# Performance work log

Hardware: AMD Instinct MI355X
Metric: run time of the kernel (lower is better)

The kernel has to match this reference:

```python
import jax, jax.numpy as jnp
import numpy as np

D_MODEL, N_HEADS, N_GROUPS, BASE = 2048, 32, 8, 10000
HEAD_DIM = D_MODEL // N_HEADS  # 64


def _rope_cache(seq, head_dim, base=BASE):
    half = head_dim // 2
    theta = 1.0 / (base ** (jnp.arange(0, head_dim, 2)[:half].astype(jnp.float32) / head_dim))
    ang = jnp.einsum('i,j->ij', jnp.arange(seq, dtype=jnp.float32), theta)  # (seq, half)
    return jnp.cos(ang), jnp.sin(ang)


def _apply_rope(x):
    # x: (b, s, h, head_dim) -> interleaved-pair rotation, matching torch module
    b, s, h, hd = x.shape
    cos, sin = _rope_cache(s, hd)
    xr = x.reshape(b, s, h, hd // 2, 2)
    c = cos[None, :, None, :]
    sn = sin[None, :, None, :]
    x0, x1 = xr[..., 0], xr[..., 1]
    out = jnp.stack((x0 * c - x1 * sn, x1 * c + x0 * sn), axis=-1)
    return out.reshape(b, s, h, hd).astype(x.dtype)


def setup_inputs() -> dict:
    key = jax.random.key(0)
    ks = jax.random.split(key, 8)
    B, S = 1, 2048
    kv_dim = HEAD_DIM * N_GROUPS
    return {
        'Q': jax.random.normal(ks[0], (B, S, D_MODEL), jnp.float32),
        'K': jax.random.normal(ks[1], (B, S, D_MODEL), jnp.float32),
        'V': jax.random.normal(ks[2], (B, S, D_MODEL), jnp.float32),
        'attention_mask': jnp.ones((B, S), jnp.int32),
        'Wq': jax.random.normal(ks[3], (D_MODEL, D_MODEL), jnp.float32) * 0.02,
        'Wk': jax.random.normal(ks[4], (D_MODEL, kv_dim), jnp.float32) * 0.02,
        'Wv': jax.random.normal(ks[5], (D_MODEL, kv_dim), jnp.float32) * 0.02,
        'Wo': jax.random.normal(ks[6], (D_MODEL, D_MODEL), jnp.float32) * 0.02,
        'bo': jnp.zeros((D_MODEL,), jnp.float32),
    }


def reference(Q, K, V, attention_mask, Wq, Wk, Wv, Wo, bo):
    b, s, _ = Q.shape
    g, hpg, hd = N_GROUPS, N_HEADS // N_GROUPS, HEAD_DIM
    # projections (weights stored as [in, out], equivalent to torch x @ W.T)
    q = (Q @ Wq).reshape(b, s, N_HEADS, hd)
    q = _apply_rope(q).reshape(b, s, g, hpg, hd)
    k = _apply_rope((K @ Wk).reshape(b, s, g, hd))
    v = (V @ Wv).reshape(b, s, g, hd)

    scale = jnp.sqrt(jnp.float32(hd))
    scores = jnp.einsum('bnghd,bmgd->bnghm', q, k) / scale  # (b, s, g, hpg, s)
    # padding mask (b, 1, 1, 1, s) and causal mask (1, s, 1, 1, s)
    pad = (attention_mask != 0)[:, None, None, None, :]
    causal = jnp.tril(jnp.ones((s, s), bool))[None, :, None, None, :]
    scores = jnp.where(pad & causal, scores, -jnp.inf)
    attn = jax.nn.softmax(scores, axis=-1)  # dropout p=0.0 -> identity
    out = jnp.einsum('bnghm,bmgd->bnghd', attn, v).reshape(b, s, D_MODEL)
    return out @ Wo + bo
```

## Files before the change

kernel.cpp:

```cpp
#include <hip/hip_runtime.h>

typedef __bf16 bf16_t;
typedef __bf16 bf16x8 __attribute__((ext_vector_type(8)));
typedef __bf16 bf16x4 __attribute__((ext_vector_type(4)));
typedef __bf16 bf16x2 __attribute__((ext_vector_type(2)));
typedef float  f32x4  __attribute__((ext_vector_type(4)));

#define LOG2E 1.44269504088896340736f

__global__ __launch_bounds__(256) void rope_table_k(float* __restrict__ cs,
                                                    float* __restrict__ sn, int S) {
  int i = blockIdx.x * 256 + threadIdx.x;
  if (i >= S * 32) return;
  int s = i >> 5, j = i & 31;
  float theta = powf(10000.0f, -(float)j * (1.0f / 32.0f));
  float a = (float)s * theta;
  cs[i] = cosf(a);
  sn[i] = sinf(a);
}

__global__ __launch_bounds__(256) void cast3_k(const float* __restrict__ A,
                                               const float* __restrict__ B,
                                               const float* __restrict__ C,
                                               bf16_t* __restrict__ oa,
                                               bf16_t* __restrict__ ob,
                                               bf16_t* __restrict__ oc) {
  const int b = blockIdx.x;
  const float* in; bf16_t* out;
  if (b < 2048) { in = A; out = oa; }
  else if (b < 4096) { in = B; out = ob; }
  else { in = C; out = oc; }
  const int j = (b & 2047) * 256 + threadIdx.x;
  const float4 v0 = *(const float4*)&in[(size_t)j * 8];
  const float4 v1 = *(const float4*)&in[(size_t)j * 8 + 4];
  bf16x8 o;
  o[0]=(bf16_t)v0.x; o[1]=(bf16_t)v0.y; o[2]=(bf16_t)v0.z; o[3]=(bf16_t)v0.w;
  o[4]=(bf16_t)v1.x; o[5]=(bf16_t)v1.y; o[6]=(bf16_t)v1.z; o[7]=(bf16_t)v1.w;
  *(bf16x8*)&out[(size_t)j * 8] = o;
}

__global__ void transpose_cast_k(const float* __restrict__ in, bf16_t* __restrict__ out,
                                 int R, int C) {
  __shared__ float tile[32][33];
  int c0 = blockIdx.x * 32, r0 = blockIdx.y * 32;
  int tx = threadIdx.x, ty = threadIdx.y;
  #pragma unroll
  for (int k = 0; k < 32; k += 8)
    tile[ty + k][tx] = in[(size_t)(r0 + ty + k) * C + c0 + tx];
  __syncthreads();
  #pragma unroll
  for (int k = 0; k < 32; k += 8)
    out[(size_t)(c0 + ty + k) * R + r0 + tx] = (bf16_t)tile[tx][ty + k];
}

__device__ __forceinline__ int xcd_swz(int bid, int nb) {
  const int q = nb >> 3, r = nb & 7;
  const int xcd = bid & 7, idx = bid >> 3;
  return (xcd < r ? xcd * (q + 1) : r * (q + 1) + (xcd - r) * q) + idx;
}

__global__ __launch_bounds__(256) void gemm2_k(
    const bf16_t* __restrict__ Aq, const bf16_t* __restrict__ Ak, const bf16_t* __restrict__ Av,
    const bf16_t* __restrict__ Bq, const bf16_t* __restrict__ Bk, const bf16_t* __restrict__ Bv,
    const int K, const int N, const int mode,
    const float* __restrict__ cs, const float* __restrict__ sn,
    bf16_t* __restrict__ oq, bf16_t* __restrict__ okg, bf16_t* __restrict__ ovt,
    float* __restrict__ ofp, const float* __restrict__ bias, const int S,
    const int ncb, const int nb) {
  __shared__ bf16_t a_lds[64][72];
  __shared__ bf16_t b_lds[128][72];
  const int tid = threadIdx.x;
  const int wid = tid >> 6, lane = tid & 63;
  const int fr = lane & 15, kg = lane >> 4;

  const int lin = xcd_swz(blockIdx.x, nb);
  const int cb = lin % ncb, rb = lin / ncb;
  const bf16_t* Ap; const bf16_t* Bp; int emode, col0;
  if (mode == 3) { Ap = Aq; Bp = Bq; emode = 3; col0 = cb * 128; }
  else if (cb < 16) { Ap = Aq; Bp = Bq; emode = 0; col0 = cb * 128; }
  else if (cb < 20) { Ap = Ak; Bp = Bk; emode = 1; col0 = (cb - 16) * 128; }
  else              { Ap = Av; Bp = Bv; emode = 2; col0 = (cb - 20) * 128; }
  const int row0 = rb * 64;
  const int wr = (wid >> 1) * 32, wc = (wid & 1) * 64;

  f32x4 acc[2][4];
  #pragma unroll
  for (int i = 0; i < 2; ++i)
    #pragma unroll
    for (int j = 0; j < 4; ++j)
      acc[i][j] = (f32x4){0.f, 0.f, 0.f, 0.f};

  const int ra = tid >> 2, sa = (tid & 3) * 16;
  const int rbv = tid >> 1, sb = (tid & 1) * 32;

  bf16x8 a0, a1, b0, b1, b2, b3;

#define LOADA(kt)                                                              \
  do {                                                                         \
    const bf16_t* p = &Ap[(size_t)(row0 + ra) * K + (kt) + sa];                \
    a0 = *(const bf16x8*)(p); a1 = *(const bf16x8*)(p + 8);                    \
    const bf16_t* q = &Bp[(size_t)(col0 + rbv) * K + (kt) + sb];               \
    b0 = *(const bf16x8*)(q);      b1 = *(const bf16x8*)(q + 8);               \
    b2 = *(const bf16x8*)(q + 16); b3 = *(const bf16x8*)(q + 24);              \
  } while (0)

  LOADA(0);

  for (int kt = 0; kt < K; kt += 64) {
    __syncthreads();
    *(bf16x8*)&a_lds[ra][sa]      = a0;
    *(bf16x8*)&a_lds[ra][sa + 8]  = a1;
    *(bf16x8*)&b_lds[rbv][sb]      = b0;
    *(bf16x8*)&b_lds[rbv][sb + 8]  = b1;
    *(bf16x8*)&b_lds[rbv][sb + 16] = b2;
    *(bf16x8*)&b_lds[rbv][sb + 24] = b3;
    __syncthreads();
    if (kt + 64 < K) LOADA(kt + 64);
    #pragma unroll
    for (int ks = 0; ks < 2; ++ks) {
      bf16x8 af[2], bfr[4];
      #pragma unroll
      for (int mi = 0; mi < 2; ++mi) af[mi]  = *(const bf16x8*)&a_lds[wr + mi * 16 + fr][ks * 32 + kg * 8];
      #pragma unroll
      for (int ni = 0; ni < 4; ++ni) bfr[ni] = *(const bf16x8*)&b_lds[wc + ni * 16 + fr][ks * 32 + kg * 8];
      #pragma unroll
      for (int mi = 0; mi < 2; ++mi)
        #pragma unroll
        for (int ni = 0; ni < 4; ++ni)
          acc[mi][ni] = __builtin_amdgcn_mfma_f32_16x16x32_bf16(af[mi], bfr[ni], acc[mi][ni], 0, 0, 0);
    }
  }
#undef LOADA

  #pragma unroll
  for (int mi = 0; mi < 2; ++mi) {
    #pragma unroll
    for (int ni = 0; ni < 4; ++ni) {
      #pragma unroll
      for (int r = 0; r < 4; ++r) {
        const int grow = row0 + wr + mi * 16 + kg * 4 + r;
        const int gcol = col0 + wc + ni * 16 + fr;
        float v = acc[mi][ni][r];
        if (emode == 3) {
          ofp[(size_t)grow * N + gcol] = v + bias[gcol];
        } else if (emode == 2) {
          const int gi = gcol >> 6, d = gcol & 63;
          ovt[((size_t)gi * 64 + d) * S + grow] = (bf16_t)v;
        } else {
          const float pv = __shfl_xor(v, 1);
          const int d = gcol & 63, p = d >> 1, hh = gcol >> 6;
          const float c = cs[grow * 32 + p], s = sn[grow * 32 + p];
          float o = (d & 1) ? fmaf(pv, s, v * c) : fmaf(-pv, s, v * c);
          if (emode == 0) {
            o *= 0.125f * LOG2E;
            oq[((size_t)hh * S + grow) * 64 + d] = (bf16_t)o;
          } else {
            okg[((size_t)hh * S + grow) * 64 + d] = (bf16_t)o;
          }
        }
      }
    }
  }
}

__device__ __forceinline__ int swz8(int r, int c) { return r * 64 + (((c) ^ (r & 7)) << 3); }

__global__ __launch_bounds__(256) void attn_k(
    const bf16_t* __restrict__ qh,
    const bf16_t* __restrict__ kgr,
    const bf16_t* __restrict__ vtg,
    const int* __restrict__ amask,
    bf16_t* __restrict__ ao,
    const int S) {
  __shared__ bf16_t k_lds[64 * 64];
  __shared__ bf16_t vt_lds[64 * 64];
  __shared__ bf16_t p_lds[4][16 * 64];
  const int tid = threadIdx.x, wid = tid >> 6, lane = tid & 63;
  const int fr = lane & 15, kgp = lane >> 4;
  const int h = blockIdx.x, g = h >> 2;
  const int qb = 31 - blockIdx.y;
  const int q0 = qb * 64 + wid * 16;
  const int qg = q0 + fr;

  const bf16_t* qbase = qh + ((size_t)h * S + q0 + fr) * 64;
  const bf16x8 qf0 = *(const bf16x8*)&qbase[kgp * 8];
  const bf16x8 qf1 = *(const bf16x8*)&qbase[32 + kgp * 8];

  f32x4 oacc[4];
  #pragma unroll
  for (int t = 0; t < 4; ++t) oacc[t] = (f32x4){0.f, 0.f, 0.f, 0.f};
  float m_ = -1e30f, l_ = 0.f;

  const int srow = tid >> 2, sc4 = tid & 3;
  const bf16_t* kbase = kgr + (size_t)g * S * 64;
  const bf16_t* vbase = vtg + (size_t)g * 64 * S;
  const int cmax = qb + 1;

  bf16x8 nk0 = *(const bf16x8*)&kbase[(size_t)srow * 64 + sc4 * 8];
  bf16x8 nk1 = *(const bf16x8*)&kbase[(size_t)srow * 64 + 32 + sc4 * 8];
  bf16x8 nv0 = *(const bf16x8*)&vbase[(size_t)srow * S + sc4 * 8];
  bf16x8 nv1 = *(const bf16x8*)&vbase[(size_t)srow * S + 32 + sc4 * 8];
  int mvc = amask[lane];
  *(bf16x8*)&k_lds[swz8(srow, sc4)]      = nk0;
  *(bf16x8*)&k_lds[swz8(srow, 4 + sc4)]  = nk1;
  *(bf16x8*)&vt_lds[swz8(srow, sc4)]     = nv0;
  *(bf16x8*)&vt_lds[swz8(srow, 4 + sc4)] = nv1;
  __syncthreads();

  for (int c = 0; c < cmax; ++c) {
    const int kc0 = c * 64;
    const unsigned long long pm = __ballot(mvc == 0);
    const bool more = (c + 1 < cmax);
    if (more) {
      const int kc1 = kc0 + 64;
      nk0 = *(const bf16x8*)&kbase[(size_t)(kc1 + srow) * 64 + sc4 * 8];
      nk1 = *(const bf16x8*)&kbase[(size_t)(kc1 + srow) * 64 + 32 + sc4 * 8];
      nv0 = *(const bf16x8*)&vbase[(size_t)srow * S + kc1 + sc4 * 8];
      nv1 = *(const bf16x8*)&vbase[(size_t)srow * S + kc1 + 32 + sc4 * 8];
      mvc = amask[kc1 + lane];
    }

    f32x4 sc[4];
    #pragma unroll
    for (int a = 0; a < 4; ++a) {
      const bf16x8 ka0 = *(const bf16x8*)&k_lds[swz8(a * 16 + fr, kgp)];
      const bf16x8 ka1 = *(const bf16x8*)&k_lds[swz8(a * 16 + fr, 4 + kgp)];
      f32x4 z = (f32x4){0.f, 0.f, 0.f, 0.f};
      z = __builtin_amdgcn_mfma_f32_16x16x32_bf16(ka0, qf0, z, 0, 0, 0);
      z = __builtin_amdgcn_mfma_f32_16x16x32_bf16(ka1, qf1, z, 0, 0, 0);
      sc[a] = z;
    }

    if (c == qb) {
      #pragma unroll
      for (int a = 0; a < 4; ++a)
        #pragma unroll
        for (int r = 0; r < 4; ++r) {
          const int kl = a * 16 + 4 * kgp + r;
          if (kc0 + kl > qg) sc[a][r] = -1e30f;
        }
    }
    if (pm) {
      #pragma unroll
      for (int a = 0; a < 4; ++a)
        #pragma unroll
        for (int r = 0; r < 4; ++r) {
          const int kl = a * 16 + 4 * kgp + r;
          if ((pm >> kl) & 1) sc[a][r] = -1e30f;
        }
    }

    float smax = sc[0][0];
    #pragma unroll
    for (int a = 0; a < 4; ++a)
      #pragma unroll
      for (int r = 0; r < 4; ++r) smax = fmaxf(smax, sc[a][r]);
    smax = fmaxf(smax, __shfl_xor(smax, 16));
    smax = fmaxf(smax, __shfl_xor(smax, 32));
    const float mn = fmaxf(m_, smax);
    const float al = exp2f(m_ - mn);
    float ps = 0.f;
    #pragma unroll
    for (int a = 0; a < 4; ++a)
      #pragma unroll
      for (int r = 0; r < 4; ++r) {
        const float p = exp2f(sc[a][r] - mn);
        sc[a][r] = p;
        ps += p;
      }
    ps += __shfl_xor(ps, 16);
    ps += __shfl_xor(ps, 32);
    l_ = l_ * al + ps;
    m_ = mn;
    #pragma unroll
    for (int t = 0; t < 4; ++t)
      #pragma unroll
      for (int r = 0; r < 4; ++r) oacc[t][r] *= al;

    #pragma unroll
    for (int a = 0; a < 4; ++a)
      #pragma unroll
      for (int j = 0; j < 2; ++j) {
        bf16x2 w;
        w[0] = (bf16_t)sc[a][2 * j];
        w[1] = (bf16_t)sc[a][2 * j + 1];
        const int off = a * 16 + 4 * kgp + 2 * j;
        *(bf16x2*)&p_lds[wid][fr * 64 + (((off >> 3) ^ (fr & 7)) << 3) + (off & 7)] = w;
      }
    const bf16x8 pa0 = *(const bf16x8*)&p_lds[wid][swz8(fr, kgp)];
    const bf16x8 pa1 = *(const bf16x8*)&p_lds[wid][swz8(fr, 4 + kgp)];

    #pragma unroll
    for (int t = 0; t < 4; ++t) {
      const bf16x8 vb0 = *(const bf16x8*)&vt_lds[swz8(t * 16 + fr, kgp)];
      const bf16x8 vb1 = *(const bf16x8*)&vt_lds[swz8(t * 16 + fr, 4 + kgp)];
      oacc[t] = __builtin_amdgcn_mfma_f32_16x16x32_bf16(vb0, pa0, oacc[t], 0, 0, 0);
      oacc[t] = __builtin_amdgcn_mfma_f32_16x16x32_bf16(vb1, pa1, oacc[t], 0, 0, 0);
    }

    if (more) {
      __syncthreads();
      *(bf16x8*)&k_lds[swz8(srow, sc4)]      = nk0;
      *(bf16x8*)&k_lds[swz8(srow, 4 + sc4)]  = nk1;
      *(bf16x8*)&vt_lds[swz8(srow, sc4)]     = nv0;
      *(bf16x8*)&vt_lds[swz8(srow, 4 + sc4)] = nv1;
      __syncthreads();
    }
  }

  const float inv = 1.0f / l_;
  #pragma unroll
  for (int t = 0; t < 4; ++t) {
    bf16x4 o4;
    #pragma unroll
    for (int r = 0; r < 4; ++r) o4[r] = (bf16_t)(oacc[t][r] * inv);
    *(bf16x4*)&ao[(size_t)(q0 + fr) * 2048 + h * 64 + t * 16 + 4 * kgp] = o4;
  }
}

extern "C" void kernel_launch(void* const* d_in, const int* in_sizes, int n_in,
                              void* d_out, int out_size, void* d_ws, size_t ws_size,
                              hipStream_t stream) {
  const float* Q  = (const float*)d_in[0];
  const float* K  = (const float*)d_in[1];
  const float* V  = (const float*)d_in[2];
  const int*   am = (const int*)d_in[3];
  const float* Wq = (const float*)d_in[4];
  const float* Wk = (const float*)d_in[5];
  const float* Wv = (const float*)d_in[6];
  const float* Wo = (const float*)d_in[7];
  const float* bo = (const float*)d_in[8];
  float* out = (float*)d_out;

  const int S = 2048, D = 2048, KV = 512;
  char* w = (char*)d_ws;
  const size_t MB = 1u << 20;
  bf16_t* WqT = (bf16_t*)(w + 0 * MB);
  bf16_t* WoT = (bf16_t*)(w + 8 * MB);
  bf16_t* WkT = (bf16_t*)(w + 16 * MB);
  bf16_t* WvT = (bf16_t*)(w + 18 * MB);
  bf16_t* qh  = (bf16_t*)(w + 20 * MB);
  bf16_t* kgr = (bf16_t*)(w + 28 * MB);
  bf16_t* vtg = (bf16_t*)(w + 30 * MB);
  bf16_t* ao  = (bf16_t*)(w + 32 * MB);
  bf16_t* Qb  = (bf16_t*)(w + 40 * MB);
  bf16_t* Kb  = (bf16_t*)(w + 48 * MB);
  bf16_t* Vb  = (bf16_t*)(w + 56 * MB);
  float*  cs  = (float*)(w + 64 * MB);
  float*  sn  = (float*)(w + 64 * MB + 256 * 1024);

  rope_table_k<<<256, 256, 0, stream>>>(cs, sn, S);
  cast3_k<<<6144, 256, 0, stream>>>(Q, K, V, Qb, Kb, Vb);
  dim3 tb(32, 8);
  transpose_cast_k<<<dim3(64, 64), tb, 0, stream>>>(Wq, WqT, D, D);
  transpose_cast_k<<<dim3(16, 64), tb, 0, stream>>>(Wk, WkT, D, KV);
  transpose_cast_k<<<dim3(16, 64), tb, 0, stream>>>(Wv, WvT, D, KV);
  transpose_cast_k<<<dim3(64, 64), tb, 0, stream>>>(Wo, WoT, D, D);

  gemm2_k<<<768, 256, 0, stream>>>(Qb, Kb, Vb, WqT, WkT, WvT, D, D, 5,
                                   cs, sn, qh, kgr, vtg, nullptr, nullptr, S, 24, 768);

  attn_k<<<dim3(32, 32), 256, 0, stream>>>(qh, kgr, vtg, am, ao, S);

  gemm2_k<<<512, 256, 0, stream>>>(ao, nullptr, nullptr, WoT, nullptr, nullptr,
                                   D, D, 3, nullptr, nullptr, nullptr, nullptr,
                                   nullptr, out, bo, S, 16, 512);
}
```

Before: 162.1 us.

## Use 128x128 tiles for QKV projection, supertile block mapping, merge weight transposes

The fused QKV projection now uses 128x128 output tiles with 4x4 MFMA fragments per wave, which halves the block count and raises operand reuse per LDS load. Both GEMMs map blocks through a 4x4 supertile order with serpentine traversal after XCD swizzling, to improve L2 locality. The output projection gets its own specialised kernel, and the four weight transposes are merged into one launch. The larger tiles raise register and LDS use and leave fewer blocks to fill the CUs.

```diff
diff --git a/kernel.cpp b/kernel.cpp
--- a/kernel.cpp
+++ b/kernel.cpp
@@ -39,10 +39,19 @@
   *(bf16x8*)&out[(size_t)j * 8] = o;
 }
 
-__global__ void transpose_cast_k(const float* __restrict__ in, bf16_t* __restrict__ out,
-                                 int R, int C) {
+__global__ void transpose4_k(const float* __restrict__ Wq, const float* __restrict__ Wk,
+                             const float* __restrict__ Wv, const float* __restrict__ Wo,
+                             bf16_t* __restrict__ WqT, bf16_t* __restrict__ WkT,
+                             bf16_t* __restrict__ WvT, bf16_t* __restrict__ WoT) {
   __shared__ float tile[32][33];
-  int c0 = blockIdx.x * 32, r0 = blockIdx.y * 32;
+  const int bx = blockIdx.x;
+  const float* in; bf16_t* out; int C, cbl;
+  if (bx < 64)      { in = Wq; out = WqT; C = 2048; cbl = bx; }
+  else if (bx < 80) { in = Wk; out = WkT; C = 512;  cbl = bx - 64; }
+  else if (bx < 96) { in = Wv; out = WvT; C = 512;  cbl = bx - 80; }
+  else              { in = Wo; out = WoT; C = 2048; cbl = bx - 96; }
+  const int R = 2048;
+  int c0 = cbl * 32, r0 = blockIdx.y * 32;
   int tx = threadIdx.x, ty = threadIdx.y;
   #pragma unroll
   for (int k = 0; k < 32; k += 8)
@@ -54,86 +63,89 @@
 }
 
 __device__ __forceinline__ int xcd_swz(int bid, int nb) {
-  const int q = nb >> 3, r = nb & 7;
-  const int xcd = bid & 7, idx = bid >> 3;
-  return (xcd < r ? xcd * (q + 1) : r * (q + 1) + (xcd - r) * q) + idx;
-}
-
-__global__ __launch_bounds__(256) void gemm2_k(
+  const int q = nb >> 3;
+  return (bid & 7) * q + (bid >> 3);
+}
+__device__ __forceinline__ void st_map(int lin, int nstc, int& rb, int& cb) {
+  const int stid = lin >> 4, w = lin & 15;
+  const int sr = stid / nstc, t = stid - sr * nstc;
+  const int sc = (sr & 1) ? (nstc - 1 - t) : t;
+  rb = sr * 4 + (w >> 2);
+  cb = sc * 4 + (w & 3);
+}
+
+__global__ __launch_bounds__(256) void gemm128_k(
     const bf16_t* __restrict__ Aq, const bf16_t* __restrict__ Ak, const bf16_t* __restrict__ Av,
     const bf16_t* __restrict__ Bq, const bf16_t* __restrict__ Bk, const bf16_t* __restrict__ Bv,
-    const int K, const int N, const int mode,
-    const float* __restrict__ cs, const float* __restrict__ sn,
-    bf16_t* __restrict__ oq, bf16_t* __restrict__ okg, bf16_t* __restrict__ ovt,
-    float* __restrict__ ofp, const float* __restrict__ bias, const int S,
-    const int ncb, const int nb) {
-  __shared__ bf16_t a_lds[64][72];
+    const int K, const float* __restrict__ cs, const float* __restrict__ sn,
+    bf16_t* __restrict__ oq, bf16_t* __restrict__ okg, bf16_t* __restrict__ ovt, const int S) {
+  __shared__ bf16_t a_lds[128][72];
   __shared__ bf16_t b_lds[128][72];
   const int tid = threadIdx.x;
   const int wid = tid >> 6, lane = tid & 63;
   const int fr = lane & 15, kg = lane >> 4;
 
-  const int lin = xcd_swz(blockIdx.x, nb);
-  const int cb = lin % ncb, rb = lin / ncb;
+  const int lin = xcd_swz(blockIdx.x, 384);
+  int rb, cb; st_map(lin, 6, rb, cb);
   const bf16_t* Ap; const bf16_t* Bp; int emode, col0;
-  if (mode == 3) { Ap = Aq; Bp = Bq; emode = 3; col0 = cb * 128; }
-  else if (cb < 16) { Ap = Aq; Bp = Bq; emode = 0; col0 = cb * 128; }
+  if (cb < 16)      { Ap = Aq; Bp = Bq; emode = 0; col0 = cb * 128; }
   else if (cb < 20) { Ap = Ak; Bp = Bk; emode = 1; col0 = (cb - 16) * 128; }
   else              { Ap = Av; Bp = Bv; emode = 2; col0 = (cb - 20) * 128; }
-  const int row0 = rb * 64;
-  const int wr = (wid >> 1) * 32, wc = (wid & 1) * 64;
-
-  f32x4 acc[2][4];
-  #pragma unroll
-  for (int i = 0; i < 2; ++i)
+  const int row0 = rb * 128;
+  const int wr = (wid >> 1) * 64, wc = (wid & 1) * 64;
+
+  f32x4 acc[4][4];
+  #pragma unroll
+  for (int i = 0; i < 4; ++i)
     #pragma unroll
     for (int j = 0; j < 4; ++j)
       acc[i][j] = (f32x4){0.f, 0.f, 0.f, 0.f};
 
-  const int ra = tid >> 2, sa = (tid & 3) * 16;
-  const int rbv = tid >> 1, sb = (tid & 1) * 32;
-
-  bf16x8 a0, a1, b0, b1, b2, b3;
-
-#define LOADA(kt)                                                              \
+  const int rw = tid >> 1, sg = (tid & 1) * 32;
+  bf16x8 a0, a1, a2, a3, b0, b1, b2, b3;
+
+#define LOADG(kt)                                                              \
   do {                                                                         \
-    const bf16_t* p = &Ap[(size_t)(row0 + ra) * K + (kt) + sa];                \
-    a0 = *(const bf16x8*)(p); a1 = *(const bf16x8*)(p + 8);                    \
-    const bf16_t* q = &Bp[(size_t)(col0 + rbv) * K + (kt) + sb];               \
-    b0 = *(const bf16x8*)(q);      b1 = *(const bf16x8*)(q + 8);               \
-    b2 = *(const bf16x8*)(q + 16); b3 = *(const bf16x8*)(q + 24);              \
+    const bf16_t* p = &Ap[(size_t)(row0 + rw) * K + (kt) + sg];                \
+    a0 = *(const bf16x8*)(p);      a1 = *(const bf16x8*)(p + 8);               \
+    a2 = *(const bf16x8*)(p + 16); a3 = *(const bf16x8*)(p + 24);              \
+    const bf16_t* q2 = &Bp[(size_t)(col0 + rw) * K + (kt) + sg];               \
+    b0 = *(const bf16x8*)(q2);      b1 = *(const bf16x8*)(q2 + 8);             \
+    b2 = *(const bf16x8*)(q2 + 16); b3 = *(const bf16x8*)(q2 + 24);            \
   } while (0)
 
-  LOADA(0);
+  LOADG(0);
 
   for (int kt = 0; kt < K; kt += 64) {
     __syncthreads();
-    *(bf16x8*)&a_lds[ra][sa]      = a0;
-    *(bf16x8*)&a_lds[ra][sa + 8]  = a1;
-    *(bf16x8*)&b_lds[rbv][sb]      = b0;
-    *(bf16x8*)&b_lds[rbv][sb + 8]  = b1;
-    *(bf16x8*)&b_lds[rbv][sb + 16] = b2;
-    *(bf16x8*)&b_lds[rbv][sb + 24] = b3;
+    *(bf16x8*)&a_lds[rw][sg]      = a0;
+    *(bf16x8*)&a_lds[rw][sg + 8]  = a1;
+    *(bf16x8*)&a_lds[rw][sg + 16] = a2;
+    *(bf16x8*)&a_lds[rw][sg + 24] = a3;
+    *(bf16x8*)&b_lds[rw][sg]      = b0;
+    *(bf16x8*)&b_lds[rw][sg + 8]  = b1;
+    *(bf16x8*)&b_lds[rw][sg + 16] = b2;
+    *(bf16x8*)&b_lds[rw][sg + 24] = b3;
     __syncthreads();
-    if (kt + 64 < K) LOADA(kt + 64);
+    if (kt + 64 < K) LOADG(kt + 64);
     #pragma unroll
     for (int ks = 0; ks < 2; ++ks) {
-      bf16x8 af[2], bfr[4];
-      #pragma unroll
-      for (int mi = 0; mi < 2; ++mi) af[mi]  = *(const bf16x8*)&a_lds[wr + mi * 16 + fr][ks * 32 + kg * 8];
+      bf16x8 af[4], bfr[4];
+      #pragma unroll
+      for (int mi = 0; mi < 4; ++mi) af[mi]  = *(const bf16x8*)&a_lds[wr + mi * 16 + fr][ks * 32 + kg * 8];
       #pragma unroll
       for (int ni = 0; ni < 4; ++ni) bfr[ni] = *(const bf16x8*)&b_lds[wc + ni * 16 + fr][ks * 32 + kg * 8];
       #pragma unroll
-      for (int mi = 0; mi < 2; ++mi)
+      for (int mi = 0; mi < 4; ++mi)
         #pragma unroll
         for (int ni = 0; ni < 4; ++ni)
           acc[mi][ni] = __builtin_amdgcn_mfma_f32_16x16x32_bf16(af[mi], bfr[ni], acc[mi][ni], 0, 0, 0);
     }
   }
-#undef LOADA
-
-  #pragma unroll
-  for (int mi = 0; mi < 2; ++mi) {
+#undef LOADG
+
+  #pragma unroll
+  for (int mi = 0; mi < 4; ++mi) {
     #pragma unroll
     for (int ni = 0; ni < 4; ++ni) {
       #pragma unroll
@@ -141,9 +153,7 @@
         const int grow = row0 + wr + mi * 16 + kg * 4 + r;
         const int gcol = col0 + wc + ni * 16 + fr;
         float v = acc[mi][ni][r];
-        if (emode == 3) {
-          ofp[(size_t)grow * N + gcol] = v + bias[gcol];
-        } else if (emode == 2) {
+        if (emode == 2) {
           const int gi = gcol >> 6, d = gcol & 63;
           ovt[((size_t)gi * 64 + d) * S + grow] = (bf16_t)v;
         } else {
@@ -158,6 +168,83 @@
             okg[((size_t)hh * S + grow) * 64 + d] = (bf16_t)o;
           }
         }
+      }
+    }
+  }
+}
+
+__global__ __launch_bounds__(256) void gemm64o_k(
+    const bf16_t* __restrict__ A, const bf16_t* __restrict__ BT,
+    const int K, const int N,
+    float* __restrict__ ofp, const float* __restrict__ bias) {
+  __shared__ bf16_t a_lds[64][72];
+  __shared__ bf16_t b_lds[128][72];
+  const int tid = threadIdx.x;
+  const int wid = tid >> 6, lane = tid & 63;
+  const int fr = lane & 15, kg = lane >> 4;
+
+  const int lin = xcd_swz(blockIdx.x, 512);
+  int rb, cb; st_map(lin, 4, rb, cb);
+  const int row0 = rb * 64, col0 = cb * 128;
+  const int wr = (wid >> 1) * 32, wc = (wid & 1) * 64;
+
+  f32x4 acc[2][4];
+  #pragma unroll
+  for (int i = 0; i < 2; ++i)
+    #pragma unroll
+    for (int j = 0; j < 4; ++j)
+      acc[i][j] = (f32x4){0.f, 0.f, 0.f, 0.f};
+
+  const int ra = tid >> 2, sa = (tid & 3) * 16;
+  const int rbv = tid >> 1, sb = (tid & 1) * 32;
+  bf16x8 a0, a1, b0, b1, b2, b3;
+
+#define LOADG(kt)                                                              \
+  do {                                                                         \
+    const bf16_t* p = &A[(size_t)(row0 + ra) * K + (kt) + sa];                 \
+    a0 = *(const bf16x8*)(p); a1 = *(const bf16x8*)(p + 8);                    \
+    const bf16_t* q2 = &BT[(size_t)(col0 + rbv) * K + (kt) + sb];              \
+    b0 = *(const bf16x8*)(q2);      b1 = *(const bf16x8*)(q2 + 8);             \
+    b2 = *(const bf16x8*)(q2 + 16); b3 = *(const bf16x8*)(q2 + 24);            \
+  } while (0)
+
+  LOADG(0);
+
+  for (int kt = 0; kt < K; kt += 64) {
+    __syncthreads();
+    *(bf16x8*)&a_lds[ra][sa]      = a0;
+    *(bf16x8*)&a_lds[ra][sa + 8]  = a1;
+    *(bf16x8*)&b_lds[rbv][sb]      = b0;
+    *(bf16x8*)&b_lds[rbv][sb + 8]  = b1;
+    *(bf16x8*)&b_lds[rbv][sb + 16] = b2;
+    *(bf16x8*)&b_lds[rbv][sb + 24] = b3;
+    __syncthreads();
+    if (kt + 64 < K) LOADG(kt + 64);
+    #pragma unroll
+    for (int ks = 0; ks < 2; ++ks) {
+      bf16x8 af[2], bfr[4];
+      #pragma unroll
+      for (int mi = 0; mi < 2; ++mi) af[mi]  = *(const bf16x8*)&a_lds[wr + mi * 16 + fr][ks * 32 + kg * 8];
+      #pragma unroll
+      for (int ni = 0; ni < 4; ++ni) bfr[ni] = *(const bf16x8*)&b_lds[wc + ni * 16 + fr][ks * 32 + kg * 8];
+      #pragma unroll
+      for (int mi = 0; mi < 2; ++mi)
+        #pragma unroll
+        for (int ni = 0; ni < 4; ++ni)
+          acc[mi][ni] = __builtin_amdgcn_mfma_f32_16x16x32_bf16(af[mi], bfr[ni], acc[mi][ni], 0, 0, 0);
+    }
+  }
+#undef LOADG
+
+  #pragma unroll
+  for (int mi = 0; mi < 2; ++mi) {
+    #pragma unroll
+    for (int ni = 0; ni < 4; ++ni) {
+      #pragma unroll
+      for (int r = 0; r < 4; ++r) {
+        const int grow = row0 + wr + mi * 16 + kg * 4 + r;
+        const int gcol = col0 + wc + ni * 16 + fr;
+        ofp[(size_t)grow * N + gcol] = acc[mi][ni][r] + bias[gcol];
       }
     }
   }
@@ -332,7 +419,7 @@
   const float* bo = (const float*)d_in[8];
   float* out = (float*)d_out;
 
-  const int S = 2048, D = 2048, KV = 512;
+  const int S = 2048, D = 2048;
   char* w = (char*)d_ws;
   const size_t MB = 1u << 20;
   bf16_t* WqT = (bf16_t*)(w + 0 * MB);
@@ -351,18 +438,12 @@
 
   rope_table_k<<<256, 256, 0, stream>>>(cs, sn, S);
   cast3_k<<<6144, 256, 0, stream>>>(Q, K, V, Qb, Kb, Vb);
-  dim3 tb(32, 8);
-  transpose_cast_k<<<dim3(64, 64), tb, 0, stream>>>(Wq, WqT, D, D);
-  transpose_cast_k<<<dim3(16, 64), tb, 0, stream>>>(Wk, WkT, D, KV);
-  transpose_cast_k<<<dim3(16, 64), tb, 0, stream>>>(Wv, WvT, D, KV);
-  transpose_cast_k<<<dim3(64, 64), tb, 0, stream>>>(Wo, WoT, D, D);
-
-  gemm2_k<<<768, 256, 0, stream>>>(Qb, Kb, Vb, WqT, WkT, WvT, D, D, 5,
-                                   cs, sn, qh, kgr, vtg, nullptr, nullptr, S, 24, 768);
+  transpose4_k<<<dim3(160, 64), dim3(32, 8), 0, stream>>>(Wq, Wk, Wv, Wo, WqT, WkT, WvT, WoT);
+
+  gemm128_k<<<384, 256, 0, stream>>>(Qb, Kb, Vb, WqT, WkT, WvT, D,
+                                     cs, sn, qh, kgr, vtg, S);
 
   attn_k<<<dim3(32, 32), 256, 0, stream>>>(qh, kgr, vtg, am, ao, S);
 
-  gemm2_k<<<512, 256, 0, stream>>>(ao, nullptr, nullptr, WoT, nullptr, nullptr,
-                                   D, D, 3, nullptr, nullptr, nullptr, nullptr,
-                                   nullptr, out, bo, S, 16, 512);
-}
+  gemm64o_k<<<512, 256, 0, stream>>>(ao, WoT, D, D, out, bo);
+}
```

Result: slower. 165.7 us (+2.2%).

## Use direct global-to-LDS loads with swizzled layout and tiled block mapping in GEMMs

Applied to the files above, without the earlier changes.

Replaces the register-staged GEMM tile loads with global_load_lds transfers into an XOR-swizzled LDS layout, removing the LDS padding and the register copy step. Adds a super-tile block ordering with snake traversal to improve L2 reuse, and makes the GEMM mode a template parameter. Also merges the four weight transpose launches into one. The software prefetch of the next K tile is dropped, so load latency is no longer overlapped with MFMA work.

```diff
diff --git a/kernel.cpp b/kernel.cpp
--- a/kernel.cpp
+++ b/kernel.cpp
@@ -7,6 +7,11 @@
 typedef float  f32x4  __attribute__((ext_vector_type(4)));
 
 #define LOG2E 1.44269504088896340736f
+
+#define GLDS(gp, lp)                                                           \
+  __builtin_amdgcn_global_load_lds(                                            \
+      (const __attribute__((address_space(1))) void*)(gp),                     \
+      (__attribute__((address_space(3))) void*)(lp), 16, 0, 0)
 
 __global__ __launch_bounds__(256) void rope_table_k(float* __restrict__ cs,
                                                     float* __restrict__ sn, int S) {
@@ -39,10 +44,19 @@
   *(bf16x8*)&out[(size_t)j * 8] = o;
 }
 
-__global__ void transpose_cast_k(const float* __restrict__ in, bf16_t* __restrict__ out,
-                                 int R, int C) {
+__global__ void transpose4_k(const float* __restrict__ Wq, const float* __restrict__ Wk,
+                             const float* __restrict__ Wv, const float* __restrict__ Wo,
+                             bf16_t* __restrict__ WqT, bf16_t* __restrict__ WkT,
+                             bf16_t* __restrict__ WvT, bf16_t* __restrict__ WoT) {
   __shared__ float tile[32][33];
-  int c0 = blockIdx.x * 32, r0 = blockIdx.y * 32;
+  const int bx = blockIdx.x;
+  const float* in; bf16_t* out; int C, cbl;
+  if (bx < 64)      { in = Wq; out = WqT; C = 2048; cbl = bx; }
+  else if (bx < 80) { in = Wk; out = WkT; C = 512;  cbl = bx - 64; }
+  else if (bx < 96) { in = Wv; out = WvT; C = 512;  cbl = bx - 80; }
+  else              { in = Wo; out = WoT; C = 2048; cbl = bx - 96; }
+  const int R = 2048;
+  int c0 = cbl * 32, r0 = blockIdx.y * 32;
   int tx = threadIdx.x, ty = threadIdx.y;
   #pragma unroll
   for (int k = 0; k < 32; k += 8)
@@ -54,29 +68,35 @@
 }
 
 __device__ __forceinline__ int xcd_swz(int bid, int nb) {
-  const int q = nb >> 3, r = nb & 7;
-  const int xcd = bid & 7, idx = bid >> 3;
-  return (xcd < r ? xcd * (q + 1) : r * (q + 1) + (xcd - r) * q) + idx;
-}
-
-__global__ __launch_bounds__(256) void gemm2_k(
+  const int q = nb >> 3;
+  return (bid & 7) * q + (bid >> 3);
+}
+__device__ __forceinline__ void st_map(int lin, int nstc, int& rb, int& cb) {
+  const int stid = lin >> 4, w = lin & 15;
+  const int sr = stid / nstc, t = stid - sr * nstc;
+  const int sc = (sr & 1) ? (nstc - 1 - t) : t;
+  rb = sr * 4 + (w >> 2);
+  cb = sc * 4 + (w & 3);
+}
+
+template<int MODE>
+__global__ __launch_bounds__(256) void gemm_glds_k(
     const bf16_t* __restrict__ Aq, const bf16_t* __restrict__ Ak, const bf16_t* __restrict__ Av,
     const bf16_t* __restrict__ Bq, const bf16_t* __restrict__ Bk, const bf16_t* __restrict__ Bv,
-    const int K, const int N, const int mode,
-    const float* __restrict__ cs, const float* __restrict__ sn,
+    const int K, const float* __restrict__ cs, const float* __restrict__ sn,
     bf16_t* __restrict__ oq, bf16_t* __restrict__ okg, bf16_t* __restrict__ ovt,
-    float* __restrict__ ofp, const float* __restrict__ bias, const int S,
-    const int ncb, const int nb) {
-  __shared__ bf16_t a_lds[64][72];
-  __shared__ bf16_t b_lds[128][72];
-  const int tid = threadIdx.x;
-  const int wid = tid >> 6, lane = tid & 63;
+    float* __restrict__ ofp, const float* __restrict__ bias, const int S) {
+  __shared__ bf16_t a_lds[64 * 64];
+  __shared__ bf16_t b_lds[128 * 64];
+  const int tid = threadIdx.x, wid = tid >> 6, lane = tid & 63;
   const int fr = lane & 15, kg = lane >> 4;
 
-  const int lin = xcd_swz(blockIdx.x, nb);
-  const int cb = lin % ncb, rb = lin / ncb;
+  constexpr int NB   = (MODE == 0) ? 768 : 512;
+  constexpr int NSTC = (MODE == 0) ? 6 : 4;
+  const int lin = xcd_swz(blockIdx.x, NB);
+  int rb, cb; st_map(lin, NSTC, rb, cb);
   const bf16_t* Ap; const bf16_t* Bp; int emode, col0;
-  if (mode == 3) { Ap = Aq; Bp = Bq; emode = 3; col0 = cb * 128; }
+  if (MODE == 1)    { Ap = Aq; Bp = Bq; emode = 3; col0 = cb * 128; }
   else if (cb < 16) { Ap = Aq; Bp = Bq; emode = 0; col0 = cb * 128; }
   else if (cb < 20) { Ap = Ak; Bp = Bk; emode = 1; col0 = (cb - 16) * 128; }
   else              { Ap = Av; Bp = Bv; emode = 2; col0 = (cb - 20) * 128; }
@@ -90,39 +110,43 @@
     for (int j = 0; j < 4; ++j)
       acc[i][j] = (f32x4){0.f, 0.f, 0.f, 0.f};
 
-  const int ra = tid >> 2, sa = (tid & 3) * 16;
-  const int rbv = tid >> 1, sb = (tid & 1) * 32;
-
-  bf16x8 a0, a1, b0, b1, b2, b3;
-
-#define LOADA(kt)                                                              \
-  do {                                                                         \
-    const bf16_t* p = &Ap[(size_t)(row0 + ra) * K + (kt) + sa];                \
-    a0 = *(const bf16x8*)(p); a1 = *(const bf16x8*)(p + 8);                    \
-    const bf16_t* q = &Bp[(size_t)(col0 + rbv) * K + (kt) + sb];               \
-    b0 = *(const bf16x8*)(q);      b1 = *(const bf16x8*)(q + 8);               \
-    b2 = *(const bf16x8*)(q + 16); b3 = *(const bf16x8*)(q + 24);              \
-  } while (0)
-
-  LOADA(0);
+  const int rloc = lane >> 3;
+  const int schunk = ((lane & 7) ^ rloc) * 8;
+  const bf16_t* gA0 = Ap + (size_t)(row0 + (wid * 2 + 0) * 8 + rloc) * K + schunk;
+  const bf16_t* gA1 = Ap + (size_t)(row0 + (wid * 2 + 1) * 8 + rloc) * K + schunk;
+  const bf16_t* gB0 = Bp + (size_t)(col0 + (wid * 4 + 0) * 8 + rloc) * K + schunk;
+  const bf16_t* gB1 = Bp + (size_t)(col0 + (wid * 4 + 1) * 8 + rloc) * K + schunk;
+  const bf16_t* gB2 = Bp + (size_t)(col0 + (wid * 4 + 2) * 8 + rloc) * K + schunk;
+  const bf16_t* gB3 = Bp + (size_t)(col0 + (wid * 4 + 3) * 8 + rloc) * K + schunk;
+  bf16_t* lA0 = &a_lds[(wid * 2 + 0) * 512];
+  bf16_t* lA1 = &a_lds[(wid * 2 + 1) * 512];
+  bf16_t* lB0 = &b_lds[(wid * 4 + 0) * 512];
+  bf16_t* lB1 = &b_lds[(wid * 4 + 1) * 512];
+  bf16_t* lB2 = &b_lds[(wid * 4 + 2) * 512];
+  bf16_t* lB3 = &b_lds[(wid * 4 + 3) * 512];
 
   for (int kt = 0; kt < K; kt += 64) {
     __syncthreads();
-    *(bf16x8*)&a_lds[ra][sa]      = a0;
-    *(bf16x8*)&a_lds[ra][sa + 8]  = a1;
-    *(bf16x8*)&b_lds[rbv][sb]      = b0;
-    *(bf16x8*)&b_lds[rbv][sb + 8]  = b1;
-    *(bf16x8*)&b_lds[rbv][sb + 16] = b2;
-    *(bf16x8*)&b_lds[rbv][sb + 24] = b3;
+    GLDS(gA0 + kt, lA0);
+    GLDS(gA1 + kt, lA1);
+    GLDS(gB0 + kt, lB0);
+    GLDS(gB1 + kt, lB1);
+    GLDS(gB2 + kt, lB2);
+    GLDS(gB3 + kt, lB3);
     __syncthreads();
-    if (kt + 64 < K) LOADA(kt + 64);
     #pragma unroll
     for (int ks = 0; ks < 2; ++ks) {
       bf16x8 af[2], bfr[4];
       #pragma unroll
-      for (int mi = 0; mi < 2; ++mi) af[mi]  = *(const bf16x8*)&a_lds[wr + mi * 16 + fr][ks * 32 + kg * 8];
-      #pragma unroll
-      for (int ni = 0; ni < 4; ++ni) bfr[ni] = *(const bf16x8*)&b_lds[wc + ni * 16 + fr][ks * 32 + kg * 8];
+      for (int mi = 0; mi < 2; ++mi) {
+        const int r = wr + mi * 16 + fr;
+        af[mi] = *(const bf16x8*)&a_lds[r * 64 + (((ks * 4 + kg) ^ (fr & 7)) * 8)];
+      }
+      #pragma unroll
+      for (int ni = 0; ni < 4; ++ni) {
+        const int r = wc + ni * 16 + fr;
+        bfr[ni] = *(const bf16x8*)&b_lds[r * 64 + (((ks * 4 + kg) ^ (fr & 7)) * 8)];
+      }
       #pragma unroll
       for (int mi = 0; mi < 2; ++mi)
         #pragma unroll
@@ -130,7 +154,6 @@
           acc[mi][ni] = __builtin_amdgcn_mfma_f32_16x16x32_bf16(af[mi], bfr[ni], acc[mi][ni], 0, 0, 0);
     }
   }
-#undef LOADA
 
   #pragma unroll
   for (int mi = 0; mi < 2; ++mi) {
@@ -142,7 +165,7 @@
         const int gcol = col0 + wc + ni * 16 + fr;
         float v = acc[mi][ni][r];
         if (emode == 3) {
-          ofp[(size_t)grow * N + gcol] = v + bias[gcol];
+          ofp[(size_t)grow * 2048 + gcol] = v + bias[gcol];
         } else if (emode == 2) {
           const int gi = gcol >> 6, d = gcol & 63;
           ovt[((size_t)gi * 64 + d) * S + grow] = (bf16_t)v;
@@ -332,7 +355,7 @@
   const float* bo = (const float*)d_in[8];
   float* out = (float*)d_out;
 
-  const int S = 2048, D = 2048, KV = 512;
+  const int S = 2048, D = 2048;
   char* w = (char*)d_ws;
   const size_t MB = 1u << 20;
   bf16_t* WqT = (bf16_t*)(w + 0 * MB);
@@ -351,18 +374,14 @@
 
   rope_table_k<<<256, 256, 0, stream>>>(cs, sn, S);
   cast3_k<<<6144, 256, 0, stream>>>(Q, K, V, Qb, Kb, Vb);
-  dim3 tb(32, 8);
-  transpose_cast_k<<<dim3(64, 64), tb, 0, stream>>>(Wq, WqT, D, D);
-  transpose_cast_k<<<dim3(16, 64), tb, 0, stream>>>(Wk, WkT, D, KV);
-  transpose_cast_k<<<dim3(16, 64), tb, 0, stream>>>(Wv, WvT, D, KV);
-  transpose_cast_k<<<dim3(64, 64), tb, 0, stream>>>(Wo, WoT, D, D);
-
-  gemm2_k<<<768, 256, 0, stream>>>(Qb, Kb, Vb, WqT, WkT, WvT, D, D, 5,
-                                   cs, sn, qh, kgr, vtg, nullptr, nullptr, S, 24, 768);
+  transpose4_k<<<dim3(160, 64), dim3(32, 8), 0, stream>>>(Wq, Wk, Wv, Wo, WqT, WkT, WvT, WoT);
+
+  gemm_glds_k<0><<<768, 256, 0, stream>>>(Qb, Kb, Vb, WqT, WkT, WvT, D,
+                                          cs, sn, qh, kgr, vtg, nullptr, nullptr, S);
 
   attn_k<<<dim3(32, 32), 256, 0, stream>>>(qh, kgr, vtg, am, ao, S);
 
-  gemm2_k<<<512, 256, 0, stream>>>(ao, nullptr, nullptr, WoT, nullptr, nullptr,
-                                   D, D, 3, nullptr, nullptr, nullptr, nullptr,
-                                   nullptr, out, bo, S, 16, 512);
-}
+  gemm_glds_k<1><<<512, 256, 0, stream>>>(ao, nullptr, nullptr, WoT, nullptr, nullptr,
+                                          D, nullptr, nullptr, nullptr, nullptr, nullptr,
+                                          out, bo, S);
+}
```

New measurement: 153.5 us. 5.3% less time.
